# Optimization experiments

Measured on AMD Instinct MI355X. Metric: run time of the kernel, lower is better.

## Reference

```python
import jax, jax.numpy as jnp
import numpy as np

B, L, N, M, E_EDGE, C = 8, 256, 1024, 8, 16384, 50
EMB, D, TDIM, ETYPES = 768, 256, 50, 50
H, DH, LAYERS = 4, 64, 2
VOCAB_W, VOCAB_E = 30000, 100000
K_SPLIT = N // 2  # fixed kg/logic node split (original uses data-dependent index)


def setup_inputs() -> dict:
    key = jax.random.key(0)
    ks = jax.random.split(key, 32)
    s = 0.02
    inp = {}
    inp["sentence"] = jax.random.randint(ks[0], (B, L), 0, VOCAB_W)
    inp["mask"] = jnp.ones((B, L), jnp.float32)
    inp["nodes"] = jax.random.randint(ks[1], (B, N, M), 0, VOCAB_E)
    inp["node_mask"] = jnp.ones((B, N, M), jnp.float32)
    inp["node_types"] = jax.random.randint(ks[2], (B, N + 1), 0, 100)
    inp["edges"] = jax.random.randint(ks[3], (B, 2, E_EDGE), 0, N + 1)
    inp["edge_types"] = jax.random.randint(ks[4], (B, E_EDGE), 0, ETYPES)
    inp["word_embed"] = jax.random.normal(ks[5], (VOCAB_W, EMB)) * s
    inp["entity_table"] = jax.random.normal(ks[6], (VOCAB_E, EMB)) * s
    inp["type_table"] = jax.random.normal(ks[7], (100, TDIM)) * s
    inp["mlp_w1"] = jax.random.normal(ks[8], (EMB, 1024)) * s
    inp["mlp_b1"] = jnp.zeros((1024,), jnp.float32)
    inp["mlp_w2"] = jax.random.normal(ks[9], (1024, EMB)) * s
    inp["mlp_b2"] = jnp.zeros((EMB,), jnp.float32)
    inp["ntw_w"] = jax.random.normal(ks[10], (EMB, EMB)) * s
    inp["proj_w"] = jax.random.normal(ks[11], (EMB, D)) * s
    inp["proj_b"] = jnp.zeros((D,), jnp.float32)
    inp["type_proj_w"] = jax.random.normal(ks[12], (TDIM, D)) * s
    inp["edge_type_table"] = jax.random.normal(ks[13], (ETYPES, TDIM)) * s
    inp["gnn_wq"] = jax.random.normal(ks[14], (LAYERS, D, D)) * s
    inp["gnn_wk"] = jax.random.normal(ks[15], (LAYERS, D, D)) * s
    inp["gnn_wv"] = jax.random.normal(ks[16], (LAYERS, D, D)) * s
    inp["gnn_we"] = jax.random.normal(ks[17], (LAYERS, TDIM, D)) * s
    inp["cls_w"] = jax.random.normal(ks[18], (EMB + 2 * D, EMB)) * s
    inp["cls_b"] = jnp.zeros((EMB,), jnp.float32)
    inp["cls2_w"] = jax.random.normal(ks[19], (C, EMB)) * s
    inp["cls2_b"] = jnp.zeros((C,), jnp.float32)
    return inp


def reference(sentence, mask, nodes, node_mask, node_types, edges, edge_types,
              word_embed, entity_table, type_table, mlp_w1, mlp_b1, mlp_w2, mlp_b2,
              ntw_w, proj_w, proj_b, type_proj_w, edge_type_table,
              gnn_wq, gnn_wk, gnn_wv, gnn_we, cls_w, cls_b, cls2_w, cls2_b):
    # PLM encoder stand-in: masked mean pool over word embeddings -> [B, EMB]
    text_vec = (word_embed[sentence] * mask[:, :, None]).sum(1) / (mask.sum(1, keepdims=True) + 1e-9)

    def per_graph(nd, nm, nt, eg, et, tv):
        ne = entity_table[nd]                                        # [N, M, EMB]
        logic = jnp.maximum(ne[K_SPLIT:] @ mlp_w1 + mlp_b1, 0.0) @ mlp_w2 + mlp_b2
        ne = jnp.concatenate([ne[:K_SPLIT], logic], axis=0)
        ne = ne @ ntw_w                                              # x @ W (no bias, no transpose)
        ne = (ne * nm[:, :, None]).sum(axis=1)                       # masked sum pool -> [N, EMB]
        h = jnp.concatenate([tv[None], ne], axis=0) @ proj_w + proj_b  # [N+1, D]
        h = h + type_table[nt] @ type_proj_w                         # inject node-type embeds
        src, dst = eg[0], eg[1]
        eemb = edge_type_table[et]                                   # [E, TDIM]
        Nn = N + 1
        for l in range(LAYERS):
            q = (h @ gnn_wq[l]).reshape(Nn, H, DH)
            k = (h @ gnn_wk[l]).reshape(Nn, H, DH)
            v = (h @ gnn_wv[l]).reshape(Nn, H, DH)
            ke = (eemb @ gnn_we[l]).reshape(E_EDGE, H, DH)
            logits = (q[dst] * (k[src] + ke)).sum(-1) / np.float32(np.sqrt(DH))  # [E, H]
            mx = jax.ops.segment_max(logits, dst, num_segments=Nn)
            ex = jnp.exp(logits - mx[dst])
            den = jax.ops.segment_sum(ex, dst, num_segments=Nn)
            alpha = ex / (den[dst] + 1e-9)
            agg = jax.ops.segment_sum(alpha[..., None] * v[src], dst, num_segments=Nn).reshape(Nn, D)
            h = jax.nn.relu(h + agg)
        return h[0], h[1:1 + C]

    ctx, lab = jax.vmap(per_graph)(nodes, node_mask, node_types, edges, edge_types, text_vec)
    ans_t = jnp.broadcast_to(ctx[:, None, :], (B, C, D))
    prompt = jnp.broadcast_to(text_vec[:, None, :], (B, C, EMB))
    pool = jnp.concatenate([ans_t, lab, prompt], axis=2) @ cls_w + cls_b   # [B, C, EMB]
    return (pool * cls2_w[None]).sum(-1) + cls2_b[None]                     # [B, C]
```

## Files before the change

kernel.cpp:

```cpp
#include <hip/hip_runtime.h>
#include <hip/hip_bf16.h>
#include <stdint.h>

using bf16 = __hip_bfloat16;
typedef __attribute__((ext_vector_type(8))) short short8;
typedef __attribute__((ext_vector_type(4))) float f32x4;
typedef __attribute__((address_space(3))) unsigned int lds_u32;
typedef const __attribute__((address_space(1))) unsigned int gbl_u32;

#define HSTRIDE 1040
#define NNODES 1025
#define EE 16384
#define MAXDEG 192

__device__ __forceinline__ bf16 f2b(float x) { return __float2bfloat16(x); }
__device__ __forceinline__ float b2f(bf16 x) { return __bfloat162float(x); }
__device__ __forceinline__ float bu2f(unsigned short u) {
    union { unsigned int i; float f; } x;
    x.i = ((unsigned int)u) << 16;
    return x.f;
}

__device__ __forceinline__ size_t midx(int row) {
    int G = row >> 3, m = row & 7, b = G >> 9;
    return (size_t)(G + 512 * (b + 1)) * 8 + m;
}

template <int EPIL>
__device__ __forceinline__ void gemm_body(const bf16* __restrict__ A, const bf16* __restrict__ Bt,
                                          bf16* __restrict__ Cb, float* __restrict__ Cf,
                                          const float* __restrict__ bias,
                                          const float* __restrict__ smr,
                                          int M, int N, int K, int NT, int swz, int bid) {
    __shared__ bf16 As[128][32];
    __shared__ bf16 Bs[128][32];
    const int tid = threadIdx.x;
    int mt, nt;
    if (swz) {
        const int MT8 = (M >> 7) >> 3;
        const int j = bid >> 3;
        mt = (bid & 7) * MT8 + j / NT;
        nt = j - (j / NT) * NT;
    } else {
        mt = bid / NT;
        nt = bid - mt * NT;
    }
    const int m0 = mt << 7;
    const int n0 = nt << 7;
    const int lane = tid & 63;
    const int wave = tid >> 6;
    const int wm = (wave >> 1) << 6;
    const int wn = (wave & 1) << 6;
    const int rsel = lane & 15;
    const int qd = lane >> 4;
    f32x4 acc[4][4];
#pragma unroll
    for (int i = 0; i < 4; i++)
#pragma unroll
        for (int jj = 0; jj < 4; jj++) acc[i][jj] = (f32x4){0.f, 0.f, 0.f, 0.f};

    const int c0 = tid, r0 = c0 >> 2, kk0 = (c0 & 3) << 3;
    const int c1 = tid + 256, r1 = c1 >> 2, kk1 = (c1 & 3) << 3;

    for (int k0 = 0; k0 < K; k0 += 32) {
        __syncthreads();
        {
            const bf16* ga0 = A + (size_t)(m0 + r0) * K + (k0 + kk0);
            __builtin_amdgcn_global_load_lds((gbl_u32*)ga0, (lds_u32*)&As[r0][kk0], 16, 0, 0);
            const bf16* ga1 = A + (size_t)(m0 + r1) * K + (k0 + kk1);
            __builtin_amdgcn_global_load_lds((gbl_u32*)ga1, (lds_u32*)&As[r1][kk1], 16, 0, 0);
            const bf16* gb0 = Bt + (size_t)(n0 + r0) * K + (k0 + kk0);
            __builtin_amdgcn_global_load_lds((gbl_u32*)gb0, (lds_u32*)&Bs[r0][kk0], 16, 0, 0);
            const bf16* gb1 = Bt + (size_t)(n0 + r1) * K + (k0 + kk1);
            __builtin_amdgcn_global_load_lds((gbl_u32*)gb1, (lds_u32*)&Bs[r1][kk1], 16, 0, 0);
        }
        __syncthreads();
        short8 af[4], bfr[4];
#pragma unroll
        for (int i = 0; i < 4; i++) af[i] = *(const short8*)&As[wm + i * 16 + rsel][qd << 3];
#pragma unroll
        for (int jj = 0; jj < 4; jj++) bfr[jj] = *(const short8*)&Bs[wn + jj * 16 + rsel][qd << 3];
#pragma unroll
        for (int i = 0; i < 4; i++)
#pragma unroll
            for (int jj = 0; jj < 4; jj++)
                acc[i][jj] = __builtin_amdgcn_mfma_f32_16x16x32_bf16(af[i], bfr[jj], acc[i][jj], 0, 0, 0);
    }
#pragma unroll
    for (int i = 0; i < 4; i++) {
        const int rbase = m0 + wm + i * 16 + (qd << 2);
        float sm4[4];
        if constexpr (EPIL == 5) {
#pragma unroll
            for (int r = 0; r < 4; r++) sm4[r] = smr[rbase + r];
        }
#pragma unroll
        for (int jj = 0; jj < 4; jj++) {
            const int col = n0 + wn + jj * 16 + rsel;
            float bv = 0.f;
            if constexpr (EPIL == 4 || EPIL == 5) bv = bias[col];
#pragma unroll
            for (int r = 0; r < 4; r++) {
                const int row = rbase + r;
                if constexpr (EPIL == 0) {
                    Cb[(size_t)row * N + col] = f2b(acc[i][jj][r]);
                } else if constexpr (EPIL == 4) {
                    const int bb = row >> 10, nn2 = row & 1023;
                    Cf[((size_t)bb * HSTRIDE + 1 + nn2) * 256 + col] = acc[i][jj][r] + bv;
                } else {
                    const int dest = row + 512 * ((row >> 9) + 1);
                    Cb[(size_t)dest * N + col] = f2b(acc[i][jj][r] + sm4[r] * bv);
                }
            }
        }
    }
}

template <int EPIL>
__global__ __launch_bounds__(256) void gemm_bt(const bf16* __restrict__ A,
                                               const bf16* __restrict__ Bt,
                                               bf16* __restrict__ Cb, float* __restrict__ Cf,
                                               const float* __restrict__ bias,
                                               const float* __restrict__ smr,
                                               int M, int N, int K, int NT, int swz) {
    gemm_body<EPIL>(A, Bt, Cb, Cf, bias, smr, M, N, K, NT, swz, blockIdx.x);
}

__device__ __forceinline__ void tr_tile(const float* __restrict__ in, bf16* __restrict__ out,
                                        int R, int C, int gx, int gy, int tid,
                                        float (*tile)[33]) {
    int tx = tid & 31, ty = tid >> 5;
    int bx = gx * 32, by = gy * 32;
    for (int i = 0; i < 32; i += 8)
        tile[ty + i][tx] = in[(size_t)(by + ty + i) * C + bx + tx];
    __syncthreads();
    for (int i = 0; i < 32; i += 8)
        out[(size_t)(bx + ty + i) * R + by + tx] = f2b(tile[tx][ty + i]);
}

__global__ __launch_bounds__(256) void k_prep(
    const float* __restrict__ mlp_w1, const float* __restrict__ mlp_w2,
    const float* __restrict__ ntw_w, const float* __restrict__ proj_w,
    const float* __restrict__ gnn_wq, const float* __restrict__ gnn_wk,
    const float* __restrict__ gnn_wv,
    const float* __restrict__ type_table, const float* __restrict__ type_proj_w,
    const float* __restrict__ edge_tt, const float* __restrict__ gnn_we,
    const float* __restrict__ cls_w, const float* __restrict__ cls2_w,
    const float* __restrict__ cls_b, const float* __restrict__ cls2_b,
    const int* __restrict__ sent, const float* __restrict__ maskp,
    const float* __restrict__ we,
    bf16* __restrict__ w1t, bf16* __restrict__ w2t, bf16* __restrict__ ntwbf,
    bf16* __restrict__ projt, bf16* __restrict__ wqkvt,
    float* __restrict__ tpe, float* __restrict__ etewe,
    float* __restrict__ weff, float* __restrict__ beff,
    float* __restrict__ tvp, float* __restrict__ msump, int* __restrict__ counts) {
    __shared__ float tile[32][33];
    int u = blockIdx.x;
    int tid = threadIdx.x;
    if (u < 768) {
        tr_tile(mlp_w1, w1t, 768, 1024, u % 32, u / 32, tid, tile);
        return;
    }
    u -= 768;
    if (u < 768) {
        tr_tile(mlp_w2, w2t, 1024, 768, u % 24, u / 24, tid, tile);
        return;
    }
    u -= 768;
    if (u < 576) {
        int base = (u * 256 + tid) * 4;
        float4 v = *(const float4*)(ntw_w + base);
        union { bf16 h[4]; uint2 q; } pk;
        pk.h[0] = f2b(v.x); pk.h[1] = f2b(v.y); pk.h[2] = f2b(v.z); pk.h[3] = f2b(v.w);
        *(uint2*)(ntwbf + base) = pk.q;
        return;
    }
    u -= 576;
    if (u < 192) {
        tr_tile(proj_w, projt, 768, 256, u % 8, u / 8, tid, tile);
        return;
    }
    u -= 192;
    if (u < 384) {
        int z = u / 64, v = u % 64;
        int l = z / 3, which = z % 3;
        const float* in = (which == 0 ? gnn_wq : which == 1 ? gnn_wk : gnn_wv) + (size_t)l * 65536;
        bf16* o = wqkvt + (size_t)l * 196608 + (size_t)which * 65536;
        tr_tile(in, o, 256, 256, v % 8, v / 8, tid, tile);
        return;
    }
    u -= 384;
    if (u < 200) {
        const float* X;
        const float* W;
        float* out;
        if (u < 100) {
            X = type_table + u * 50; W = type_proj_w; out = tpe + u * 256;
        } else if (u < 150) {
            X = edge_tt + (u - 100) * 50; W = gnn_we; out = etewe + (u - 100) * 256;
        } else {
            X = edge_tt + (u - 150) * 50; W = gnn_we + 12800; out = etewe + 12800 + (u - 150) * 256;
        }
        float acc = 0.f;
        for (int k = 0; k < 50; k++) acc += X[k] * W[k * 256 + tid];
        out[tid] = acc;
        return;
    }
    u -= 200;
    if (u < 320) {
        int wave = tid >> 6, lane = tid & 63;
        int k = u * 4 + wave;
        float wrow[12];
#pragma unroll
        for (int t = 0; t < 12; t++) wrow[t] = cls_w[(size_t)k * 768 + t * 64 + lane];
        for (int c = 0; c < 50; c++) {
            const float* c2 = cls2_w + c * 768;
            float acc = 0.f;
#pragma unroll
            for (int t = 0; t < 12; t++) acc += wrow[t] * c2[t * 64 + lane];
            for (int s = 32; s > 0; s >>= 1) acc += __shfl_xor(acc, s, 64);
            if (lane == 0) weff[c * 1280 + k] = acc;
        }
        if (u == 0) {
            float brow[12];
#pragma unroll
            for (int t = 0; t < 12; t++) brow[t] = cls_b[t * 64 + lane];
            for (int c = wave; c < 50; c += 4) {
                const float* c2 = cls2_w + c * 768;
                float acc = 0.f;
#pragma unroll
                for (int t = 0; t < 12; t++) acc += brow[t] * c2[t * 64 + lane];
                for (int s = 32; s > 0; s >>= 1) acc += __shfl_xor(acc, s, 64);
                if (lane == 0) beff[c] = acc + cls2_b[c];
            }
        }
        return;
    }
    u -= 320;
    if (u < 64) {
        int b = u >> 3, ch = u & 7;
        float a0 = 0.f, a1 = 0.f, a2 = 0.f, ms = 0.f;
        for (int l = ch * 32; l < ch * 32 + 32; l++) {
            int w = sent[b * 256 + l];
            float mm = maskp[b * 256 + l];
            const float* row = we + (size_t)w * 768;
            a0 += mm * row[tid];
            a1 += mm * row[tid + 256];
            a2 += mm * row[tid + 512];
            ms += mm;
        }
        float* dst = tvp + (size_t)(b * 8 + ch) * 768;
        dst[tid] = a0;
        dst[tid + 256] = a1;
        dst[tid + 512] = a2;
        if (tid == 0) msump[b * 8 + ch] = ms;
        return;
    }
    u -= 64;
    {
        int i = u * 256 + tid;
        if (i < 8 * NNODES) counts[i] = 0;
    }
}

__global__ __launch_bounds__(256) void k_mid(
    const bf16* __restrict__ projt, const bf16* __restrict__ ntwbf, bf16* __restrict__ wnpt,
    const float* __restrict__ tvp, const float* __restrict__ msump, float* __restrict__ tv,
    const float* __restrict__ node_mask, float* __restrict__ summask,
    const int* __restrict__ edges, int* __restrict__ counts) {
    int u = blockIdx.x;
    int tid = threadIdx.x;
    if (u < 12) {
        gemm_body<0>(projt, ntwbf, wnpt, nullptr, nullptr, nullptr, 256, 768, 768, 6, 0, u);
        return;
    }
    u -= 12;
    if (u < 8) {
        int b = u;
        float ms = 0.f;
        for (int p = 0; p < 8; p++) ms += msump[b * 8 + p];
        float inv = 1.f / (ms + 1e-9f);
        float a0 = 0.f, a1 = 0.f, a2 = 0.f;
        for (int p = 0; p < 8; p++) {
            const float* s = tvp + (size_t)(b * 8 + p) * 768;
            a0 += s[tid];
            a1 += s[tid + 256];
            a2 += s[tid + 512];
        }
        tv[b * 768 + tid] = a0 * inv;
        tv[b * 768 + tid + 256] = a1 * inv;
        tv[b * 768 + tid + 512] = a2 * inv;
        return;
    }
    u -= 8;
    if (u < 16) {
        int G = u * 256 + tid;
        if (G < 4096) {
            int b = G >> 9;
            const float* p = node_mask + (size_t)(G + 512 * (b + 1)) * 8;
            float s = 0.f;
            for (int m = 0; m < 8; m++) s += p[m];
            summask[G] = s;
        }
        return;
    }
    u -= 16;
    {
        int flat = u * 256 + tid;
        int b = flat >> 14, e = flat & (EE - 1);
        int d = edges[b * 2 * EE + EE + e];
        atomicAdd(&counts[b * NNODES + d], 1);
    }
}

__global__ __launch_bounds__(256) void k_mlp1_scan(
    const int* __restrict__ nodes, const float* __restrict__ ent,
    const bf16* __restrict__ Bt, const float* __restrict__ b1,
    const float* __restrict__ node_mask, bf16* __restrict__ pooledh,
    const int* __restrict__ counts, int* __restrict__ offs, int* __restrict__ cursor) {
    __shared__ bf16 As[128][32];
    __shared__ bf16 Bs[128][32];
    __shared__ int tsum[256];
    const int tid = threadIdx.x;
    const int bid = blockIdx.x;
    if (bid >= 2048) {
        int b = bid - 2048, t = tid;
        int beg = t * 5;
        int end = beg + 5;
        if (end > NNODES) end = NNODES;
        int cl[5];
        int s = 0;
        for (int i = beg; i < end; i++) {
            int v = counts[b * NNODES + i];
            cl[i - beg] = v;
            s += v;
        }
        tsum[t] = s;
        __syncthreads();
        for (int d = 1; d < 256; d <<= 1) {
            int v = tsum[t];
            int vo = (t >= d) ? tsum[t - d] : 0;
            __syncthreads();
            tsum[t] = v + vo;
            __syncthreads();
        }
        int run = (t == 0) ? 0 : tsum[t - 1];
        for (int i = beg; i < end; i++) {
            offs[b * 1026 + i] = run;
            cursor[b * NNODES + i] = run;
            run += cl[i - beg];
        }
        if (beg == NNODES) offs[b * 1026 + NNODES] = run;
        return;
    }
    const int j = bid >> 3;
    const int m0 = (((bid & 7) * 32) + (j >> 3)) << 7;
    const int n0 = (j & 7) << 7;
    const int lane = tid & 63;
    const int wave = tid >> 6;
    const int wm = (wave >> 1) << 6;
    const int wn = (wave & 1) << 6;
    const int rsel = lane & 15;
    const int qd = lane >> 4;
    const int K = 768;

    const float* arow[4];
    int rl_row = tid >> 3;
    int piece4 = (tid & 7) << 2;
#pragma unroll
    for (int p = 0; p < 4; p++) {
        int grow = m0 + p * 32 + rl_row;
        int id = nodes[midx(grow)];
        arow[p] = ent + (size_t)id * 768 + piece4;
    }

    f32x4 acc[4][4];
#pragma unroll
    for (int i = 0; i < 4; i++)
#pragma unroll
        for (int jj = 0; jj < 4; jj++) acc[i][jj] = (f32x4){0.f, 0.f, 0.f, 0.f};

    const int c0 = tid, r0 = c0 >> 2, kk0 = (c0 & 3) << 3;
    const int c1 = tid + 256, r1 = c1 >> 2, kk1 = (c1 & 3) << 3;

    for (int k0 = 0; k0 < K; k0 += 32) {
        __syncthreads();
        const bf16* gb0 = Bt + (size_t)(n0 + r0) * K + (k0 + kk0);
        __builtin_amdgcn_global_load_lds((gbl_u32*)gb0, (lds_u32*)&Bs[r0][kk0], 16, 0, 0);
        const bf16* gb1 = Bt + (size_t)(n0 + r1) * K + (k0 + kk1);
        __builtin_amdgcn_global_load_lds((gbl_u32*)gb1, (lds_u32*)&Bs[r1][kk1], 16, 0, 0);
#pragma unroll
        for (int p = 0; p < 4; p++) {
            float4 v = *(const float4*)(arow[p] + k0);
            union { bf16 h[4]; uint2 u; } pk;
            pk.h[0] = f2b(v.x); pk.h[1] = f2b(v.y); pk.h[2] = f2b(v.z); pk.h[3] = f2b(v.w);
            *(uint2*)&As[p * 32 + rl_row][piece4] = pk.u;
        }
        __syncthreads();
        short8 af[4], bfr[4];
#pragma unroll
        for (int i = 0; i < 4; i++) af[i] = *(const short8*)&As[wm + i * 16 + rsel][qd << 3];
#pragma unroll
        for (int jj = 0; jj < 4; jj++) bfr[jj] = *(const short8*)&Bs[wn + jj * 16 + rsel][qd << 3];
#pragma unroll
        for (int i = 0; i < 4; i++)
#pragma unroll
            for (int jj = 0; jj < 4; jj++)
                acc[i][jj] = __builtin_amdgcn_mfma_f32_16x16x32_bf16(af[i], bfr[jj], acc[i][jj], 0, 0, 0);
    }
#pragma unroll
    for (int i = 0; i < 4; i++) {
        const int rbase = m0 + wm + i * 16 + (qd << 2);
        float w4[4];
#pragma unroll
        for (int r = 0; r < 4; r++) w4[r] = node_mask[midx(rbase + r)];
        const int Gout = (m0 + wm + i * 16 + ((qd & 2) << 2)) >> 3;
#pragma unroll
        for (int jj = 0; jj < 4; jj++) {
            const int col = n0 + wn + jj * 16 + rsel;
            const float bv = b1[col];
            float s = 0.f;
#pragma unroll
            for (int r = 0; r < 4; r++) s += w4[r] * fmaxf(acc[i][jj][r] + bv, 0.f);
            s += __shfl_xor(s, 16, 64);
            if ((qd & 1) == 0) pooledh[(size_t)Gout * 1024 + col] = f2b(s);
        }
    }
}

__global__ __launch_bounds__(256) void k_mega4(
    const bf16* __restrict__ pooledh, const bf16* __restrict__ w2t, bf16* __restrict__ pooled,
    const float* __restrict__ mlp_b2, const float* __restrict__ summask,
    const int* __restrict__ nodes, const float* __restrict__ nmask, const float* __restrict__ ent,
    const float* __restrict__ tv, const float* __restrict__ proj_w, float* __restrict__ hp) {
    int u = blockIdx.x;
    int tid = threadIdx.x;
    if (u < 192) {
        gemm_body<5>(pooledh, w2t, pooled, nullptr, mlp_b2, summask, 4096, 768, 1024, 6, 1, u);
        return;
    }
    u -= 192;
    if (u < 4096) {
        int b = u >> 9, n = u & 511;
        int base = (((b << 10) + n) << 3);
        float a0 = 0.f, a1 = 0.f, a2 = 0.f;
        for (int m = 0; m < 8; m++) {
            float w = nmask[base + m];
            const float* row = ent + (size_t)nodes[base + m] * 768;
            a0 += w * row[tid];
            a1 += w * row[tid + 256];
            a2 += w * row[tid + 512];
        }
        bf16* dst = pooled + (size_t)((b << 10) + n) * 768;
        dst[tid] = f2b(a0);
        dst[tid + 256] = f2b(a1);
        dst[tid + 512] = f2b(a2);
        return;
    }
    u -= 4096;
    {
        int b = u / 6, kc = u % 6;
        float acc = 0.f;
        for (int k = kc * 128; k < kc * 128 + 128; k++)
            acc += tv[b * 768 + k] * proj_w[k * 256 + tid];
        hp[(size_t)(b * 6 + kc) * 256 + tid] = acc;
    }
}

__global__ __launch_bounds__(256) void k_mega5(
    const bf16* __restrict__ pooled, const bf16* __restrict__ wnpt,
    float* __restrict__ h, const float* __restrict__ proj_b,
    const int* __restrict__ edges, int* __restrict__ cursor, int* __restrict__ eord) {
    int u = blockIdx.x;
    int tid = threadIdx.x;
    if (u < 128) {
        gemm_body<4>(pooled, wnpt, nullptr, h, proj_b, nullptr, 8192, 256, 768, 2, 1, u);
        return;
    }
    u -= 128;
    {
        int flat = u * 256 + tid;
        int b = flat >> 14, e = flat & (EE - 1);
        int d = edges[b * 2 * EE + EE + e];
        int pos = atomicAdd(&cursor[b * NNODES + d], 1);
        eord[b * EE + pos] = e;
    }
}

__global__ __launch_bounds__(256) void k_tpe_add(const int* __restrict__ ntypes,
                                                 const float* __restrict__ tpe,
                                                 const float* __restrict__ hp,
                                                 const float* __restrict__ proj_b,
                                                 float* __restrict__ h, bf16* __restrict__ hbf) {
    int i = blockIdx.x;
    int b = blockIdx.y;
    int c = threadIdx.x;
    size_t idx = ((size_t)b * HSTRIDE + i) * 256 + c;
    if (i < NNODES) {
        int t = ntypes[b * NNODES + i];
        float v;
        if (i == 0) {
            v = proj_b[c];
            for (int p = 0; p < 6; p++) v += hp[(size_t)(b * 6 + p) * 256 + c];
        } else {
            v = h[idx];
        }
        v += tpe[t * 256 + c];
        h[idx] = v;
        hbf[idx] = f2b(v);
    } else {
        h[idx] = 0.f;
        hbf[idx] = f2b(0.f);
    }
}

__global__ __launch_bounds__(256) void k_gnn_node(const int* __restrict__ edges,
                                                  const int* __restrict__ etypes,
                                                  const int* __restrict__ offs,
                                                  const int* __restrict__ eord,
                                                  const float* __restrict__ etewe,
                                                  const bf16* __restrict__ qkv,
                                                  float* __restrict__ h, bf16* __restrict__ hbf) {
    int bid = blockIdx.x;
    int b = bid / NNODES, n = bid % NNODES;
    int o0 = offs[b * 1026 + n];
    int deg = offs[b * 1026 + n + 1] - o0;
    if (deg > MAXDEG) deg = MAXDEG;
    int tid = threadIdx.x, lane = tid & 63, wave = tid >> 6;
    __shared__ float qs[256];
    __shared__ float elog[MAXDEG][4];
    __shared__ int srcs[MAXDEG];
    __shared__ float smax[4], sden[4];
    __shared__ float vpart[4][256];
    size_t qbase = ((size_t)(b * HSTRIDE + n)) * 768;
    qs[tid] = b2f(qkv[qbase + tid]);
    __syncthreads();
    for (int i = wave; i < deg; i += 4) {
        int e = eord[b * EE + o0 + i];
        int src = edges[b * 2 * EE + e];
        int et = etypes[b * EE + e];
        const bf16* krow = qkv + ((size_t)(b * HSTRIDE + src)) * 768 + 256;
        const float* kerow = etewe + et * 256;
        float sum[4];
#pragma unroll
        for (int hh = 0; hh < 4; hh++) {
            float v = qs[hh * 64 + lane] * (b2f(krow[hh * 64 + lane]) + kerow[hh * 64 + lane]);
            for (int s = 32; s > 0; s >>= 1) v += __shfl_xor(v, s, 64);
            sum[hh] = v;
        }
        if (lane == 0) {
            srcs[i] = src;
#pragma unroll
            for (int hh = 0; hh < 4; hh++) elog[i][hh] = sum[hh] * 0.125f;
        }
    }
    __syncthreads();
    if (deg > 0) {
        int hh = wave;
        float m = -1e30f;
        for (int i = lane; i < deg; i += 64) m = fmaxf(m, elog[i][hh]);
        for (int s = 32; s > 0; s >>= 1) m = fmaxf(m, __shfl_xor(m, s, 64));
        float den = 0.f;
        for (int i = lane; i < deg; i += 64) den += expf(elog[i][hh] - m);
        for (int s = 32; s > 0; s >>= 1) den += __shfl_xor(den, s, 64);
        if (lane == 0) { smax[hh] = m; sden[hh] = den; }
    }
    __syncthreads();
    for (int i = tid; i < deg; i += 256) {
#pragma unroll
        for (int hh = 0; hh < 4; hh++)
            elog[i][hh] = expf(elog[i][hh] - smax[hh]) / (sden[hh] + 1e-9f);
    }
    __syncthreads();
    float a0 = 0.f, a1 = 0.f, a2 = 0.f, a3 = 0.f;
    const int hsel = lane >> 4;
    for (int i = wave; i < deg; i += 4) {
        float w = elog[i][hsel];
        const bf16* vrow = qkv + ((size_t)(b * HSTRIDE + srcs[i])) * 768 + 512 + lane * 4;
        ushort4 uu = *reinterpret_cast<const ushort4*>(vrow);
        a0 += w * bu2f(uu.x);
        a1 += w * bu2f(uu.y);
        a2 += w * bu2f(uu.z);
        a3 += w * bu2f(uu.w);
    }
    vpart[wave][lane * 4 + 0] = a0;
    vpart[wave][lane * 4 + 1] = a1;
    vpart[wave][lane * 4 + 2] = a2;
    vpart[wave][lane * 4 + 3] = a3;
    __syncthreads();
    float acc = vpart[0][tid] + vpart[1][tid] + vpart[2][tid] + vpart[3][tid];
    size_t hidx = ((size_t)(b * HSTRIDE + n)) * 256 + tid;
    float v = fmaxf(h[hidx] + acc, 0.f);
    h[hidx] = v;
    hbf[hidx] = f2b(v);
}

__global__ __launch_bounds__(256) void k_cls(const float* __restrict__ h,
                                             const float* __restrict__ tv,
                                             const float* __restrict__ weff,
                                             const float* __restrict__ beff,
                                             float* __restrict__ out) {
    int bc = blockIdx.x;
    int b = bc / 50, c = bc % 50;
    int tid = threadIdx.x;
    const float* we = weff + c * 1280;
    float acc = 0.f;
    for (int kk = tid; kk < 1280; kk += 256) {
        float f;
        if (kk < 256) f = h[((size_t)(b * HSTRIDE)) * 256 + kk];
        else if (kk < 512) f = h[((size_t)(b * HSTRIDE + 1 + c)) * 256 + (kk - 256)];
        else f = tv[b * 768 + (kk - 512)];
        acc += f * we[kk];
    }
    __shared__ float red[256];
    red[tid] = acc;
    __syncthreads();
    for (int s = 128; s > 0; s >>= 1) {
        if (tid < s) red[tid] += red[tid + s];
        __syncthreads();
    }
    if (tid == 0) out[b * 50 + c] = red[0] + beff[c];
}

extern "C" void kernel_launch(void* const* d_in, const int* in_sizes, int n_in,
                              void* d_out, int out_size, void* d_ws, size_t ws_size,
                              hipStream_t stream) {
    (void)in_sizes; (void)n_in; (void)out_size; (void)ws_size;
    const int* sentence       = (const int*)d_in[0];
    const float* mask         = (const float*)d_in[1];
    const int* nodes          = (const int*)d_in[2];
    const float* node_mask    = (const float*)d_in[3];
    const int* node_types     = (const int*)d_in[4];
    const int* edges          = (const int*)d_in[5];
    const int* edge_types     = (const int*)d_in[6];
    const float* word_embed   = (const float*)d_in[7];
    const float* entity_table = (const float*)d_in[8];
    const float* type_table   = (const float*)d_in[9];
    const float* mlp_w1       = (const float*)d_in[10];
    const float* mlp_b1       = (const float*)d_in[11];
    const float* mlp_w2       = (const float*)d_in[12];
    const float* mlp_b2       = (const float*)d_in[13];
    const float* ntw_w        = (const float*)d_in[14];
    const float* proj_w       = (const float*)d_in[15];
    const float* proj_b       = (const float*)d_in[16];
    const float* type_proj_w  = (const float*)d_in[17];
    const float* edge_tt      = (const float*)d_in[18];
    const float* gnn_wq       = (const float*)d_in[19];
    const float* gnn_wk       = (const float*)d_in[20];
    const float* gnn_wv       = (const float*)d_in[21];
    const float* gnn_we       = (const float*)d_in[22];
    const float* cls_w        = (const float*)d_in[23];
    const float* cls_b        = (const float*)d_in[24];
    const float* cls2_w       = (const float*)d_in[25];
    const float* cls2_b       = (const float*)d_in[26];

    char* ws = (char*)d_ws;
    size_t off = 0;
    auto alloc = [&](size_t bytes) {
        size_t r = off;
        off += (bytes + 255) & ~((size_t)255);
        return r;
    };
    bf16* w1t     = (bf16*)(ws + alloc((size_t)1024 * 768 * 2));
    bf16* w2t     = (bf16*)(ws + alloc((size_t)768 * 1024 * 2));
    bf16* ntwbf   = (bf16*)(ws + alloc((size_t)768 * 768 * 2));
    bf16* projt   = (bf16*)(ws + alloc((size_t)256 * 768 * 2));
    bf16* wnpt    = (bf16*)(ws + alloc((size_t)256 * 768 * 2));
    bf16* wqkvt   = (bf16*)(ws + alloc((size_t)2 * 768 * 256 * 2));
    float* tpe    = (float*)(ws + alloc((size_t)100 * 256 * 4));
    float* etewe  = (float*)(ws + alloc((size_t)2 * 50 * 256 * 4));
    float* weff   = (float*)(ws + alloc((size_t)50 * 1280 * 4));
    float* beff   = (float*)(ws + alloc(256));
    float* tv     = (float*)(ws + alloc((size_t)8 * 768 * 4));
    float* tvp    = (float*)(ws + alloc((size_t)64 * 768 * 4));
    float* msump  = (float*)(ws + alloc((size_t)64 * 4));
    float* hp     = (float*)(ws + alloc((size_t)48 * 256 * 4));
    float* summask= (float*)(ws + alloc((size_t)4096 * 4));
    int* counts   = (int*)(ws + alloc((size_t)8 * NNODES * 4));
    int* offs     = (int*)(ws + alloc((size_t)8 * 1026 * 4));
    int* cursor   = (int*)(ws + alloc((size_t)8 * NNODES * 4));
    int* eord     = (int*)(ws + alloc((size_t)8 * EE * 4));
    bf16* pooledh = (bf16*)(ws + alloc((size_t)4096 * 1024 * 2));
    bf16* pooled  = (bf16*)(ws + alloc((size_t)8192 * 768 * 2));
    float* h      = (float*)(ws + alloc((size_t)8 * HSTRIDE * 256 * 4));
    bf16* hbf     = (bf16*)(ws + alloc((size_t)8 * HSTRIDE * 256 * 2));
    bf16* qkv     = (bf16*)(ws + alloc((size_t)8 * HSTRIDE * 768 * 2));

    k_prep<<<3305, 256, 0, stream>>>(mlp_w1, mlp_w2, ntw_w, proj_w, gnn_wq, gnn_wk, gnn_wv,
                                     type_table, type_proj_w, edge_tt, gnn_we,
                                     cls_w, cls2_w, cls_b, cls2_b,
                                     sentence, mask, word_embed,
                                     w1t, w2t, ntwbf, projt, wqkvt,
                                     tpe, etewe, weff, beff, tvp, msump, counts);
    k_mid<<<548, 256, 0, stream>>>(projt, ntwbf, wnpt, tvp, msump, tv,
                                   node_mask, summask, edges, counts);
    k_mlp1_scan<<<2056, 256, 0, stream>>>(nodes, entity_table, w1t, mlp_b1, node_mask, pooledh,
                                          counts, offs, cursor);
    k_mega4<<<4336, 256, 0, stream>>>(pooledh, w2t, pooled, mlp_b2, summask,
                                      nodes, node_mask, entity_table, tv, proj_w, hp);
    k_mega5<<<640, 256, 0, stream>>>(pooled, wnpt, h, proj_b, edges, cursor, eord);
    k_tpe_add<<<dim3(1040, 8), 256, 0, stream>>>(node_types, tpe, hp, proj_b, h, hbf);

    for (int l = 0; l < 2; l++) {
        gemm_bt<0><<<390, 256, 0, stream>>>(hbf, wqkvt + l * 196608, qkv, nullptr, nullptr,
                                            nullptr, 8320, 768, 256, 6, 0);
        k_gnn_node<<<8 * NNODES, 256, 0, stream>>>(edges, edge_types, offs, eord,
                                                   etewe + l * 12800, qkv, h, hbf);
    }
    k_cls<<<400, 256, 0, stream>>>(h, tv, weff, beff, (float*)d_out);
}
```

Before: 804.5 us.

## Pre-gather entity rows to bf16, fuse type-embed add into projection epilogue, vectorize edge logits

Entity-row gathering and fp32-to-bf16 conversion move out of the MLP1 GEMM into k_prep. They are written to a new 32768x768 bf16 buffer that the GEMM then streams with global_load_lds. The logic-node pooling moves from k_mega4 to k_prep, and the edge bucketing moves from k_mega5 to k_mega4. The projection GEMM epilogue now adds the type embedding and writes both the fp32 and bf16 h, which removes the separate k_tpe_add pass over all nodes. The GNN edge-logit loop now loads 4 elements per lane with a 16-lane shuffle reduction instead of four 64-lane reductions. In exchange there is an extra materialized 48MB bf16 buffer and a larger prep kernel.

Result: faster. 749.4 us (-6.8%).

```diff
diff --git a/kernel.cpp b/kernel.cpp
--- a/kernel.cpp
+++ b/kernel.cpp
@@ -31,6 +31,9 @@
                                           bf16* __restrict__ Cb, float* __restrict__ Cf,
                                           const float* __restrict__ bias,
                                           const float* __restrict__ smr,
+                                          const int* __restrict__ nty,
+                                          const float* __restrict__ tpe,
+                                          bf16* __restrict__ hbf2,
                                           int M, int N, int K, int NT, int swz, int bid) {
     __shared__ bf16 As[128][32];
     __shared__ bf16 Bs[128][32];
@@ -90,23 +93,35 @@
     for (int i = 0; i < 4; i++) {
         const int rbase = m0 + wm + i * 16 + (qd << 2);
         float sm4[4];
+        int t4[4];
         if constexpr (EPIL == 5) {
 #pragma unroll
             for (int r = 0; r < 4; r++) sm4[r] = smr[rbase + r];
+        }
+        if constexpr (EPIL == 6) {
+#pragma unroll
+            for (int r = 0; r < 4; r++) {
+                const int row = rbase + r;
+                const int bb = row >> 10, nn2 = row & 1023;
+                t4[r] = nty[bb * NNODES + 1 + nn2];
+            }
         }
 #pragma unroll
         for (int jj = 0; jj < 4; jj++) {
             const int col = n0 + wn + jj * 16 + rsel;
             float bv = 0.f;
-            if constexpr (EPIL == 4 || EPIL == 5) bv = bias[col];
+            if constexpr (EPIL == 5 || EPIL == 6) bv = bias[col];
 #pragma unroll
             for (int r = 0; r < 4; r++) {
                 const int row = rbase + r;
                 if constexpr (EPIL == 0) {
                     Cb[(size_t)row * N + col] = f2b(acc[i][jj][r]);
-                } else if constexpr (EPIL == 4) {
+                } else if constexpr (EPIL == 6) {
                     const int bb = row >> 10, nn2 = row & 1023;
-                    Cf[((size_t)bb * HSTRIDE + 1 + nn2) * 256 + col] = acc[i][jj][r] + bv;
+                    float v = acc[i][jj][r] + bv + tpe[t4[r] * 256 + col];
+                    size_t ix = ((size_t)bb * HSTRIDE + 1 + nn2) * 256 + col;
+                    Cf[ix] = v;
+                    hbf2[ix] = f2b(v);
                 } else {
                     const int dest = row + 512 * ((row >> 9) + 1);
                     Cb[(size_t)dest * N + col] = f2b(acc[i][jj][r] + sm4[r] * bv);
@@ -123,7 +138,8 @@
                                                const float* __restrict__ bias,
                                                const float* __restrict__ smr,
                                                int M, int N, int K, int NT, int swz) {
-    gemm_body<EPIL>(A, Bt, Cb, Cf, bias, smr, M, N, K, NT, swz, blockIdx.x);
+    gemm_body<EPIL>(A, Bt, Cb, Cf, bias, smr, nullptr, nullptr, nullptr, M, N, K, NT, swz,
+                    blockIdx.x);
 }
 
 __device__ __forceinline__ void tr_tile(const float* __restrict__ in, bf16* __restrict__ out,
@@ -139,6 +155,8 @@
 }
 
 __global__ __launch_bounds__(256) void k_prep(
+    const int* __restrict__ nodes, const float* __restrict__ node_mask,
+    const float* __restrict__ ent, bf16* __restrict__ Abf, bf16* __restrict__ pooled,
     const float* __restrict__ mlp_w1, const float* __restrict__ mlp_w2,
     const float* __restrict__ ntw_w, const float* __restrict__ proj_w,
     const float* __restrict__ gnn_wq, const float* __restrict__ gnn_wk,
@@ -157,6 +175,41 @@
     __shared__ float tile[32][33];
     int u = blockIdx.x;
     int tid = threadIdx.x;
+    if (u < 4096) {
+        int G = u;
+        int r = tid >> 5, lane32 = tid & 31;
+        int id = nodes[midx(G * 8 + r)];
+        const float* src = ent + (size_t)id * 768;
+        bf16* dst = Abf + (size_t)(G * 8 + r) * 768;
+#pragma unroll
+        for (int p = 0; p < 6; p++) {
+            int col = p * 128 + lane32 * 4;
+            float4 v = *(const float4*)(src + col);
+            union { bf16 h[4]; uint2 q; } pk;
+            pk.h[0] = f2b(v.x); pk.h[1] = f2b(v.y); pk.h[2] = f2b(v.z); pk.h[3] = f2b(v.w);
+            *(uint2*)(dst + col) = pk.q;
+        }
+        return;
+    }
+    u -= 4096;
+    if (u < 4096) {
+        int b = u >> 9, n = u & 511;
+        int base = (((b << 10) + n) << 3);
+        float a0 = 0.f, a1 = 0.f, a2 = 0.f;
+        for (int m = 0; m < 8; m++) {
+            float w = node_mask[base + m];
+            const float* row = ent + (size_t)nodes[base + m] * 768;
+            a0 += w * row[tid];
+            a1 += w * row[tid + 256];
+            a2 += w * row[tid + 512];
+        }
+        bf16* dst = pooled + (size_t)((b << 10) + n) * 768;
+        dst[tid] = f2b(a0);
+        dst[tid + 256] = f2b(a1);
+        dst[tid + 512] = f2b(a2);
+        return;
+    }
+    u -= 4096;
     if (u < 768) {
         tr_tile(mlp_w1, w1t, 768, 1024, u % 32, u / 32, tid, tile);
         return;
@@ -271,7 +324,8 @@
     int u = blockIdx.x;
     int tid = threadIdx.x;
     if (u < 12) {
-        gemm_body<0>(projt, ntwbf, wnpt, nullptr, nullptr, nullptr, 256, 768, 768, 6, 0, u);
+        gemm_body<0>(projt, ntwbf, wnpt, nullptr, nullptr, nullptr, nullptr, nullptr, nullptr,
+                     256, 768, 768, 6, 0, u);
         return;
     }
     u -= 12;
@@ -314,8 +368,7 @@
 }
 
 __global__ __launch_bounds__(256) void k_mlp1_scan(
-    const int* __restrict__ nodes, const float* __restrict__ ent,
-    const bf16* __restrict__ Bt, const float* __restrict__ b1,
+    const bf16* __restrict__ Abf, const bf16* __restrict__ Bt, const float* __restrict__ b1,
     const float* __restrict__ node_mask, bf16* __restrict__ pooledh,
     const int* __restrict__ counts, int* __restrict__ offs, int* __restrict__ cursor) {
     __shared__ bf16 As[128][32];
@@ -364,16 +417,6 @@
     const int qd = lane >> 4;
     const int K = 768;
 
-    const float* arow[4];
-    int rl_row = tid >> 3;
-    int piece4 = (tid & 7) << 2;
-#pragma unroll
-    for (int p = 0; p < 4; p++) {
-        int grow = m0 + p * 32 + rl_row;
-        int id = nodes[midx(grow)];
-        arow[p] = ent + (size_t)id * 768 + piece4;
-    }
-
     f32x4 acc[4][4];
 #pragma unroll
     for (int i = 0; i < 4; i++)
@@ -385,17 +428,14 @@
 
     for (int k0 = 0; k0 < K; k0 += 32) {
         __syncthreads();
+        const bf16* ga0 = Abf + (size_t)(m0 + r0) * K + (k0 + kk0);
+        __builtin_amdgcn_global_load_lds((gbl_u32*)ga0, (lds_u32*)&As[r0][kk0], 16, 0, 0);
+        const bf16* ga1 = Abf + (size_t)(m0 + r1) * K + (k0 + kk1);
+        __builtin_amdgcn_global_load_lds((gbl_u32*)ga1, (lds_u32*)&As[r1][kk1], 16, 0, 0);
         const bf16* gb0 = Bt + (size_t)(n0 + r0) * K + (k0 + kk0);
         __builtin_amdgcn_global_load_lds((gbl_u32*)gb0, (lds_u32*)&Bs[r0][kk0], 16, 0, 0);
         const bf16* gb1 = Bt + (size_t)(n0 + r1) * K + (k0 + kk1);
         __builtin_amdgcn_global_load_lds((gbl_u32*)gb1, (lds_u32*)&Bs[r1][kk1], 16, 0, 0);
-#pragma unroll
-        for (int p = 0; p < 4; p++) {
-            float4 v = *(const float4*)(arow[p] + k0);
-            union { bf16 h[4]; uint2 u; } pk;
-            pk.h[0] = f2b(v.x); pk.h[1] = f2b(v.y); pk.h[2] = f2b(v.z); pk.h[3] = f2b(v.w);
-            *(uint2*)&As[p * 32 + rl_row][piece4] = pk.u;
-        }
         __syncthreads();
         short8 af[4], bfr[4];
 #pragma unroll
@@ -431,53 +471,25 @@
 __global__ __launch_bounds__(256) void k_mega4(
     const bf16* __restrict__ pooledh, const bf16* __restrict__ w2t, bf16* __restrict__ pooled,
     const float* __restrict__ mlp_b2, const float* __restrict__ summask,
-    const int* __restrict__ nodes, const float* __restrict__ nmask, const float* __restrict__ ent,
-    const float* __restrict__ tv, const float* __restrict__ proj_w, float* __restrict__ hp) {
+    const float* __restrict__ tv, const float* __restrict__ proj_w, float* __restrict__ hp,
+    const int* __restrict__ edges, int* __restrict__ cursor, int* __restrict__ eord) {
     int u = blockIdx.x;
     int tid = threadIdx.x;
     if (u < 192) {
-        gemm_body<5>(pooledh, w2t, pooled, nullptr, mlp_b2, summask, 4096, 768, 1024, 6, 1, u);
+        gemm_body<5>(pooledh, w2t, pooled, nullptr, mlp_b2, summask, nullptr, nullptr, nullptr,
+                     4096, 768, 1024, 6, 1, u);
         return;
     }
     u -= 192;
-    if (u < 4096) {
-        int b = u >> 9, n = u & 511;
-        int base = (((b << 10) + n) << 3);
-        float a0 = 0.f, a1 = 0.f, a2 = 0.f;
-        for (int m = 0; m < 8; m++) {
-            float w = nmask[base + m];
-            const float* row = ent + (size_t)nodes[base + m] * 768;
-            a0 += w * row[tid];
-            a1 += w * row[tid + 256];
-            a2 += w * row[tid + 512];
-        }
-        bf16* dst = pooled + (size_t)((b << 10) + n) * 768;
-        dst[tid] = f2b(a0);
-        dst[tid + 256] = f2b(a1);
-        dst[tid + 512] = f2b(a2);
-        return;
-    }
-    u -= 4096;
-    {
+    if (u < 48) {
         int b = u / 6, kc = u % 6;
         float acc = 0.f;
         for (int k = kc * 128; k < kc * 128 + 128; k++)
             acc += tv[b * 768 + k] * proj_w[k * 256 + tid];
         hp[(size_t)(b * 6 + kc) * 256 + tid] = acc;
-    }
-}
-
-__global__ __launch_bounds__(256) void k_mega5(
-    const bf16* __restrict__ pooled, const bf16* __restrict__ wnpt,
-    float* __restrict__ h, const float* __restrict__ proj_b,
-    const int* __restrict__ edges, int* __restrict__ cursor, int* __restrict__ eord) {
-    int u = blockIdx.x;
-    int tid = threadIdx.x;
-    if (u < 128) {
-        gemm_body<4>(pooled, wnpt, nullptr, h, proj_b, nullptr, 8192, 256, 768, 2, 1, u);
-        return;
-    }
-    u -= 128;
+        return;
+    }
+    u -= 48;
     {
         int flat = u * 256 + tid;
         int b = flat >> 14, e = flat & (EE - 1);
@@ -487,30 +499,33 @@
     }
 }
 
-__global__ __launch_bounds__(256) void k_tpe_add(const int* __restrict__ ntypes,
-                                                 const float* __restrict__ tpe,
-                                                 const float* __restrict__ hp,
-                                                 const float* __restrict__ proj_b,
-                                                 float* __restrict__ h, bf16* __restrict__ hbf) {
-    int i = blockIdx.x;
-    int b = blockIdx.y;
-    int c = threadIdx.x;
-    size_t idx = ((size_t)b * HSTRIDE + i) * 256 + c;
-    if (i < NNODES) {
-        int t = ntypes[b * NNODES + i];
+__global__ __launch_bounds__(256) void k_mega5(
+    const bf16* __restrict__ pooled, const bf16* __restrict__ wnpt,
+    float* __restrict__ h, bf16* __restrict__ hbf, const float* __restrict__ proj_b,
+    const int* __restrict__ ntypes, const float* __restrict__ tpe,
+    const float* __restrict__ hp) {
+    int u = blockIdx.x;
+    int tid = threadIdx.x;
+    if (u < 128) {
+        gemm_body<6>(pooled, wnpt, nullptr, h, proj_b, nullptr, ntypes, tpe, hbf,
+                     8192, 256, 768, 2, 1, u);
+        return;
+    }
+    u -= 128;
+    {
+        int b = u >> 4, ii = u & 15;
+        int i = (ii == 0) ? 0 : 1024 + ii;
+        size_t idx = ((size_t)b * HSTRIDE + i) * 256 + tid;
         float v;
-        if (i == 0) {
-            v = proj_b[c];
-            for (int p = 0; p < 6; p++) v += hp[(size_t)(b * 6 + p) * 256 + c];
+        if (ii == 0) {
+            v = proj_b[tid];
+            for (int p = 0; p < 6; p++) v += hp[(size_t)(b * 6 + p) * 256 + tid];
+            v += tpe[ntypes[b * NNODES] * 256 + tid];
         } else {
-            v = h[idx];
-        }
-        v += tpe[t * 256 + c];
+            v = 0.f;
+        }
         h[idx] = v;
         hbf[idx] = f2b(v);
-    } else {
-        h[idx] = 0.f;
-        hbf[idx] = f2b(0.f);
     }
 }
 
@@ -535,24 +550,27 @@
     size_t qbase = ((size_t)(b * HSTRIDE + n)) * 768;
     qs[tid] = b2f(qkv[qbase + tid]);
     __syncthreads();
+    const int hq = lane >> 4;
+    const int e4 = lane & 15;
+    float qreg[4];
+#pragma unroll
+    for (int j2 = 0; j2 < 4; j2++) qreg[j2] = qs[hq * 64 + e4 * 4 + j2];
     for (int i = wave; i < deg; i += 4) {
         int e = eord[b * EE + o0 + i];
         int src = edges[b * 2 * EE + e];
         int et = etypes[b * EE + e];
-        const bf16* krow = qkv + ((size_t)(b * HSTRIDE + src)) * 768 + 256;
-        const float* kerow = etewe + et * 256;
-        float sum[4];
-#pragma unroll
-        for (int hh = 0; hh < 4; hh++) {
-            float v = qs[hh * 64 + lane] * (b2f(krow[hh * 64 + lane]) + kerow[hh * 64 + lane]);
-            for (int s = 32; s > 0; s >>= 1) v += __shfl_xor(v, s, 64);
-            sum[hh] = v;
-        }
-        if (lane == 0) {
-            srcs[i] = src;
-#pragma unroll
-            for (int hh = 0; hh < 4; hh++) elog[i][hh] = sum[hh] * 0.125f;
-        }
+        const bf16* krow = qkv + ((size_t)(b * HSTRIDE + src)) * 768 + 256 + hq * 64 + e4 * 4;
+        const float* kerow = etewe + et * 256 + hq * 64 + e4 * 4;
+        ushort4 ku = *(const ushort4*)krow;
+        float4 ke = *(const float4*)kerow;
+        float v = qreg[0] * (bu2f(ku.x) + ke.x) + qreg[1] * (bu2f(ku.y) + ke.y) +
+                  qreg[2] * (bu2f(ku.z) + ke.z) + qreg[3] * (bu2f(ku.w) + ke.w);
+        v += __shfl_xor(v, 1, 64);
+        v += __shfl_xor(v, 2, 64);
+        v += __shfl_xor(v, 4, 64);
+        v += __shfl_xor(v, 8, 64);
+        if (e4 == 0) elog[i][hq] = v * 0.125f;
+        if (lane == 0) srcs[i] = src;
     }
     __syncthreads();
     if (deg > 0) {
@@ -680,26 +698,27 @@
     int* offs     = (int*)(ws + alloc((size_t)8 * 1026 * 4));
     int* cursor   = (int*)(ws + alloc((size_t)8 * NNODES * 4));
     int* eord     = (int*)(ws + alloc((size_t)8 * EE * 4));
+    bf16* Abf     = (bf16*)(ws + alloc((size_t)32768 * 768 * 2));
     bf16* pooledh = (bf16*)(ws + alloc((size_t)4096 * 1024 * 2));
     bf16* pooled  = (bf16*)(ws + alloc((size_t)8192 * 768 * 2));
     float* h      = (float*)(ws + alloc((size_t)8 * HSTRIDE * 256 * 4));
     bf16* hbf     = (bf16*)(ws + alloc((size_t)8 * HSTRIDE * 256 * 2));
     bf16* qkv     = (bf16*)(ws + alloc((size_t)8 * HSTRIDE * 768 * 2));
 
-    k_prep<<<3305, 256, 0, stream>>>(mlp_w1, mlp_w2, ntw_w, proj_w, gnn_wq, gnn_wk, gnn_wv,
-                                     type_table, type_proj_w, edge_tt, gnn_we,
-                                     cls_w, cls2_w, cls_b, cls2_b,
-                                     sentence, mask, word_embed,
-                                     w1t, w2t, ntwbf, projt, wqkvt,
-                                     tpe, etewe, weff, beff, tvp, msump, counts);
+    k_prep<<<11497, 256, 0, stream>>>(nodes, node_mask, entity_table, Abf, pooled,
+                                      mlp_w1, mlp_w2, ntw_w, proj_w, gnn_wq, gnn_wk, gnn_wv,
+                                      type_table, type_proj_w, edge_tt, gnn_we,
+                                      cls_w, cls2_w, cls_b, cls2_b,
+                                      sentence, mask, word_embed,
+                                      w1t, w2t, ntwbf, projt, wqkvt,
+                                      tpe, etewe, weff, beff, tvp, msump, counts);
     k_mid<<<548, 256, 0, stream>>>(projt, ntwbf, wnpt, tvp, msump, tv,
                                    node_mask, summask, edges, counts);
-    k_mlp1_scan<<<2056, 256, 0, stream>>>(nodes, entity_table, w1t, mlp_b1, node_mask, pooledh,
+    k_mlp1_scan<<<2056, 256, 0, stream>>>(Abf, w1t, mlp_b1, node_mask, pooledh,
                                           counts, offs, cursor);
-    k_mega4<<<4336, 256, 0, stream>>>(pooledh, w2t, pooled, mlp_b2, summask,
-                                      nodes, node_mask, entity_table, tv, proj_w, hp);
-    k_mega5<<<640, 256, 0, stream>>>(pooled, wnpt, h, proj_b, edges, cursor, eord);
-    k_tpe_add<<<dim3(1040, 8), 256, 0, stream>>>(node_types, tpe, hp, proj_b, h, hbf);
+    k_mega4<<<752, 256, 0, stream>>>(pooledh, w2t, pooled, mlp_b2, summask,
+                                     tv, proj_w, hp, edges, cursor, eord);
+    k_mega5<<<256, 256, 0, stream>>>(pooled, wnpt, h, hbf, proj_b, node_types, tpe, hp);
 
     for (int l = 0; l < 2; l++) {
         gemm_bt<0><<<390, 256, 0, stream>>>(hbf, wqkvt + l * 196608, qkv, nullptr, nullptr,
```
